# Performance work log

Measured on AMD Instinct MI355X. Metric: run time of the kernel, lower is better.

## Reference

```python
import jax, jax.numpy as jnp
import numpy as np

B, T, H, L, O = 64, 256, 1024, 4, 1024
LN_EPS = 1e-5


def setup_inputs() -> dict:
    key = jax.random.key(0)
    ks = jax.random.split(key, 8)
    s = 1.0 / np.sqrt(H)
    return {
        "inputs": jax.random.normal(ks[0], (B, T, H), jnp.float32),
        "Wx": jax.random.normal(ks[1], (L, H, H), jnp.float32) * s,   # torch Linear weight [out,in]
        "bx": jax.random.normal(ks[2], (L, H), jnp.float32) * s,
        "Wh": jax.random.normal(ks[3], (L, H, H), jnp.float32) * s,   # bias=False
        "ln_g": jnp.ones((L, H), jnp.float32),
        "ln_b": jnp.zeros((L, H), jnp.float32),
        "Wy": jax.random.normal(ks[4], (O, H), jnp.float32) * s,
        "by": jax.random.normal(ks[5], (O,), jnp.float32) * s,
    }


def _layernorm(z, g, b):
    mu = jnp.mean(z, axis=-1, keepdims=True)
    var = jnp.mean(jnp.square(z - mu), axis=-1, keepdims=True)
    return (z - mu) * jax.lax.rsqrt(var + LN_EPS) * g + b


def _forward(inputs, Wx, bx, Wh, ln_g, ln_b, Wy, by):
    x = inputs                                  # [B, T, H]
    n_layers = Wx.shape[0]
    for l in range(n_layers):
        Wx_l, bx_l, Wh_l = Wx[l], bx[l], Wh[l]
        g_l, b_l = ln_g[l], ln_b[l]

        def step(h, x_t):
            # h_t = tanh(LN(x_t Wx^T + bx + h Wh^T))  (dropout off in eval)
            z = x_t @ Wx_l.T + bx_l + h @ Wh_l.T
            h_new = jnp.tanh(_layernorm(z, g_l, b_l))
            return h_new, h_new

        h0 = jnp.zeros((x.shape[0], Wh_l.shape[0]), x.dtype)
        _, hs = jax.lax.scan(step, h0, jnp.swapaxes(x, 0, 1))  # hs: [T, B, H]
        x = jnp.swapaxes(hs, 0, 1)                              # [B, T, H]
    y = x @ Wy.T + by                                           # [B, T, O]
    return x, y


def reference(inputs, Wx, bx, Wh, ln_g, ln_b, Wy, by):
    return _forward(inputs, Wx, bx, Wh, ln_g, ln_b, Wy, by)
```

## Files before the change

### kernel.cpp

```cpp
#include <hip/hip_runtime.h>
#include <stdint.h>

#define B_ 64
#define T_ 256
#define H_ 1024
#define L_ 4
#define O_ 1024
#define LN_EPS 1e-5f
#define RING_Z 4
#define POLL_CAP (1 << 20)

typedef short v8s __attribute__((ext_vector_type(8)));
typedef float v4f __attribute__((ext_vector_type(4)));
typedef unsigned long long u64t;

__device__ __forceinline__ unsigned short f2bf(float f) {
  union { float f; unsigned u; } v; v.f = f;
  unsigned r = (v.u + 0x7FFFu + ((v.u >> 16) & 1u)) >> 16;
  return (unsigned short)r;
}
__device__ __forceinline__ float bf2f(unsigned short u) {
  union { unsigned u; float f; } v; v.u = ((unsigned)u) << 16; return v.f;
}
__device__ __forceinline__ float tanh_fast(float x) {
  float e = __expf(2.0f * x);
  return 1.0f - 2.0f / (e + 1.0f);
}

__device__ __forceinline__ int hswz(int row, int kq) {
  return ((row << 7) + ((kq ^ (kq >> 4) ^ row) & 127)) << 3;
}

__device__ __forceinline__ void poll_ge(const int* p, int v) {
  int it = 0;
  while (__hip_atomic_load(p, __ATOMIC_RELAXED, __HIP_MEMORY_SCOPE_AGENT) < v) {
    __builtin_amdgcn_s_sleep(1);
    if (++it > POLL_CAP) break;
  }
}

__global__ void k_f2b(const float* __restrict__ src, unsigned short* __restrict__ dst, int n4) {
  int i = blockIdx.x * blockDim.x + threadIdx.x;
  int stride = gridDim.x * blockDim.x;
  for (; i < n4; i += stride) {
    float4 v = *(const float4*)(src + 4 * (size_t)i);
    union { unsigned short u[4]; uint2 q; } p;
    p.u[0] = f2bf(v.x); p.u[1] = f2bf(v.y); p.u[2] = f2bf(v.z); p.u[3] = f2bf(v.w);
    *(uint2*)(dst + 4 * (size_t)i) = p.q;
  }
}

__global__ void k_prep_x(const float* __restrict__ in, unsigned short* __restrict__ X) {
  int row = blockIdx.x;
  int b = row >> 8, t = row & 255;
  const float* src = in + (size_t)row * H_;
  unsigned short* dst = X + ((size_t)t * B_ + b) * H_;
  for (int j = threadIdx.x; j < H_ / 4; j += blockDim.x) {
    float4 v = *(const float4*)(src + 4 * j);
    union { unsigned short u[4]; uint2 q; } p;
    p.u[0] = f2bf(v.x); p.u[1] = f2bf(v.y); p.u[2] = f2bf(v.z); p.u[3] = f2bf(v.w);
    *(uint2*)(dst + 4 * j) = p.q;
  }
}

__launch_bounds__(256, 2)
__global__ void k_gemm32(const float* __restrict__ Xf,
                         const unsigned short* __restrict__ Wb,
                         const float* __restrict__ bias,
                         float* __restrict__ Cout) {
  __shared__ short As[128][40];
  __shared__ short Bs[128][40];
  int bm = blockIdx.x >> 3, bn = blockIdx.x & 7;
  int row0 = bm * 128, col0 = bn * 128;
  int tid = threadIdx.x, lane = tid & 63, w = tid >> 6;
  int wm = w >> 1, wn = w & 1;
  int m15 = lane & 15, quad = lane >> 4;
  v4f acc[4][4];
  #pragma unroll
  for (int a = 0; a < 4; ++a)
    #pragma unroll
    for (int b = 0; b < 4; ++b) acc[a][b] = (v4f){0.f, 0.f, 0.f, 0.f};

  int srow = tid >> 1, sseg = tid & 1;
  const float* gA = Xf + (size_t)(row0 + srow) * 1024 + sseg * 16;
  const unsigned short* gB = Wb + (size_t)(col0 + srow) * 1024 + sseg * 16;

  for (int kb = 0; kb < 32; ++kb) {
    float4 f0 = *(const float4*)(gA + kb * 32);
    float4 f1 = *(const float4*)(gA + kb * 32 + 4);
    float4 f2 = *(const float4*)(gA + kb * 32 + 8);
    float4 f3 = *(const float4*)(gA + kb * 32 + 12);
    v8s a0, a1;
    a0[0] = (short)f2bf(f0.x); a0[1] = (short)f2bf(f0.y); a0[2] = (short)f2bf(f0.z); a0[3] = (short)f2bf(f0.w);
    a0[4] = (short)f2bf(f1.x); a0[5] = (short)f2bf(f1.y); a0[6] = (short)f2bf(f1.z); a0[7] = (short)f2bf(f1.w);
    a1[0] = (short)f2bf(f2.x); a1[1] = (short)f2bf(f2.y); a1[2] = (short)f2bf(f2.z); a1[3] = (short)f2bf(f2.w);
    a1[4] = (short)f2bf(f3.x); a1[5] = (short)f2bf(f3.y); a1[6] = (short)f2bf(f3.z); a1[7] = (short)f2bf(f3.w);
    v8s b0 = *(const v8s*)(gB + kb * 32);
    v8s b1 = *(const v8s*)(gB + kb * 32 + 8);
    *(v8s*)&As[srow][sseg * 16]     = a0;
    *(v8s*)&As[srow][sseg * 16 + 8] = a1;
    *(v8s*)&Bs[srow][sseg * 16]     = b0;
    *(v8s*)&Bs[srow][sseg * 16 + 8] = b1;
    __syncthreads();
    v8s af[4], bfr[4];
    #pragma unroll
    for (int mt = 0; mt < 4; ++mt) af[mt]  = *(v8s*)&As[wm * 64 + mt * 16 + m15][quad * 8];
    #pragma unroll
    for (int nt = 0; nt < 4; ++nt) bfr[nt] = *(v8s*)&Bs[wn * 64 + nt * 16 + m15][quad * 8];
    #pragma unroll
    for (int mt = 0; mt < 4; ++mt)
      #pragma unroll
      for (int nt = 0; nt < 4; ++nt)
        acc[mt][nt] = __builtin_amdgcn_mfma_f32_16x16x32_bf16(af[mt], bfr[nt], acc[mt][nt], 0, 0, 0);
    __syncthreads();
  }
  #pragma unroll
  for (int mt = 0; mt < 4; ++mt) {
    #pragma unroll
    for (int nt = 0; nt < 4; ++nt) {
      int col = col0 + wn * 64 + nt * 16 + m15;
      float bv = bias[col];
      #pragma unroll
      for (int r = 0; r < 4; ++r) {
        int row = row0 + wm * 64 + mt * 16 + quad * 4 + r;
        Cout[(size_t)row * 1024 + col] = acc[mt][nt][r] + bv;
      }
    }
  }
}

__launch_bounds__(256, 1)
__global__ void k_fused(const unsigned short* __restrict__ Whb_all,
                        const unsigned short* __restrict__ Wxb_all,
                        const float* __restrict__ bx_all,
                        const float* __restrict__ lng_all,
                        const float* __restrict__ lnb_all,
                        unsigned short* Xl,
                        float* Zr,
                        int* fz,
                        float* __restrict__ outx)
{
  __shared__ short hs[16 * 1024];
  __shared__ float sG[1024], sB[1024];

  const int tid = threadIdx.x, lane = tid & 63, w = tid >> 6;
  const int bid = blockIdx.x;
  const int l = bid >> 6, rb = (bid >> 4) & 3, cb = bid & 15;
  const int r0 = rb * 16, c0 = cb * 64;
  const int m15 = lane & 15, quad = lane >> 4;
  const int myrow = 4 * w + quad;
  const int chunk = m15;
  const int colg = c0 + w * 16 + m15;

  for (int i = tid; i < 1024; i += 256) { sG[i] = lng_all[l * H_ + i]; sB[i] = lnb_all[l * H_ + i]; }

  v8s bh[32];
  {
    const unsigned short* wr = Whb_all + ((size_t)l * H_ + colg) * H_ + quad * 8;
    #pragma unroll
    for (int ks = 0; ks < 32; ++ks) bh[ks] = *(const v8s*)(wr + ks * 32);
  }

  const float bias = bx_all[l * H_ + colg];
  const unsigned short* wxb = Wxb_all + ((size_t)l * H_ + colg) * H_ + quad * 8;
  int* myfz = fz + ((l * 64 + rb * 16 + cb) << 5);
  const int* peer_fz = fz + ((l * 64 + rb * 16 + chunk) << 5);
  const int* prev_fz = (l > 0) ? fz + (((l - 1) * 64 + rb * 16 + chunk) << 5) : (const int*)nullptr;

  const size_t TBH = (size_t)T_ * B_ * H_;
  const unsigned short* Xin = Xl + (size_t)l * TBH;
  unsigned short* Xout = (l < L_ - 1) ? Xl + (size_t)(l + 1) * TBH : (unsigned short*)nullptr;
  float* Zl = Zr + (size_t)l * RING_Z * 4 * 16 * 1024;

  if (l > 0) poll_ge(prev_fz, 2);
  __syncthreads();
  v4f acc = (v4f){bias, bias, bias, bias};
  {
    const unsigned short* xr = Xin + ((size_t)r0 + m15) * H_ + quad * 8;
    #pragma unroll 1
    for (int kb = 0; kb < 4; ++kb) {
      #pragma unroll
      for (int k8 = 0; k8 < 8; ++k8) {
        int ks = kb * 8 + k8;
        v8s a = *(const v8s*)(xr + ks * 32);
        v8s b = *(const v8s*)(wxb + ks * 32);
        acc = __builtin_amdgcn_mfma_f32_16x16x32_bf16(a, b, acc, 0, 0, 0);
      }
    }
  }

  for (int t = 0; t < T_; ++t) {
    float* zo = Zl + (size_t)((t & (RING_Z - 1)) * 4 + rb) * 16 * 1024;
    #pragma unroll
    for (int r = 0; r < 4; ++r)
      __hip_atomic_store(&zo[(size_t)(quad * 4 + r) * H_ + colg], acc[r],
                         __ATOMIC_RELAXED, __HIP_MEMORY_SCOPE_AGENT);
    __syncthreads();
    if (tid == 0)
      __hip_atomic_store(myfz, t + 1, __ATOMIC_RELAXED, __HIP_MEMORY_SCOPE_AGENT);

    if (t < T_ - 1) {
      if (l > 0) poll_ge(prev_fz, t + 3);
      __syncthreads();
      acc = (v4f){bias, bias, bias, bias};
      const unsigned short* xr = Xin + ((size_t)(t + 1) * B_ + r0 + m15) * H_ + quad * 8;
      #pragma unroll 1
      for (int kb = 0; kb < 4; ++kb) {
        #pragma unroll
        for (int k8 = 0; k8 < 8; ++k8) {
          int ks = kb * 8 + k8;
          v8s a = *(const v8s*)(xr + ks * 32);
          v8s b = *(const v8s*)(wxb + ks * 32);
          acc = __builtin_amdgcn_mfma_f32_16x16x32_bf16(a, b, acc, 0, 0, 0);
        }
      }
    }

    poll_ge(peer_fz, t + 1);
    const u64t* zp = (const u64t*)(zo + (size_t)myrow * H_ + chunk * 64);
    float2 zr2[32];
    #pragma unroll
    for (int j = 0; j < 32; ++j) {
      union { u64t u; float2 f; } cv;
      cv.u = __hip_atomic_load(zp + j, __ATOMIC_RELAXED, __HIP_MEMORY_SCOPE_AGENT);
      zr2[j] = cv.f;
    }
    float s = 0.f, s2 = 0.f;
    #pragma unroll
    for (int j = 0; j < 32; ++j) {
      s  += zr2[j].x + zr2[j].y;
      s2 += zr2[j].x * zr2[j].x + zr2[j].y * zr2[j].y;
    }
    #pragma unroll
    for (int m = 1; m < 16; m <<= 1) { s += __shfl_xor(s, m); s2 += __shfl_xor(s2, m); }
    float mu = s * (1.f / 1024.f);
    float var = s2 * (1.f / 1024.f) - mu * mu;
    float rs = rsqrtf(var + LN_EPS);
    #pragma unroll
    for (int g8 = 0; g8 < 8; ++g8) {
      v8s hp;
      #pragma unroll
      for (int e = 0; e < 8; ++e) {
        int cg = chunk * 64 + g8 * 8 + e;
        float zv = (e & 1) ? zr2[g8 * 4 + (e >> 1)].y : zr2[g8 * 4 + (e >> 1)].x;
        float hv = tanh_fast((zv - mu) * rs * sG[cg] + sB[cg]);
        hp[e] = (short)f2bf(hv);
      }
      *(v8s*)&hs[hswz(myrow, chunk * 8 + g8)] = hp;
    }
    __syncthreads();

    {
      int row = tid >> 4, ci = tid & 15;
      int colbase = c0 + ci * 4;
      const short* hp = &hs[hswz(row, colbase >> 3) + (ci & 1) * 4];
      union { unsigned short u[4]; u64t q; } pk;
      pk.u[0] = (unsigned short)hp[0]; pk.u[1] = (unsigned short)hp[1];
      pk.u[2] = (unsigned short)hp[2]; pk.u[3] = (unsigned short)hp[3];
      if (l < L_ - 1) {
        u64t* xdst = (u64t*)(Xout + ((size_t)t * B_ + r0 + row) * H_ + colbase);
        __hip_atomic_store(xdst, pk.q, __ATOMIC_RELAXED, __HIP_MEMORY_SCOPE_AGENT);
      } else {
        float4 f;
        f.x = bf2f(pk.u[0]); f.y = bf2f(pk.u[1]); f.z = bf2f(pk.u[2]); f.w = bf2f(pk.u[3]);
        *(float4*)(outx + ((size_t)(r0 + row) * T_ + t) * H_ + colbase) = f;
      }
    }
    if (t < T_ - 1) {
      #pragma unroll
      for (int ks = 0; ks < 32; ++ks) {
        v8s a = *(const v8s*)&hs[hswz(m15, ks * 4 + quad)];
        acc = __builtin_amdgcn_mfma_f32_16x16x32_bf16(a, bh[ks], acc, 0, 0, 0);
      }
    }
  }
  __syncthreads();
  if (tid == 0)
    __hip_atomic_store(myfz, T_ + 1, __ATOMIC_RELAXED, __HIP_MEMORY_SCOPE_AGENT);
}

extern "C" void kernel_launch(void* const* d_in, const int* in_sizes, int n_in,
                              void* d_out, int out_size, void* d_ws, size_t ws_size,
                              hipStream_t stream) {
  const float* inp = (const float*)d_in[0];
  const float* Wx  = (const float*)d_in[1];
  const float* bx  = (const float*)d_in[2];
  const float* Wh  = (const float*)d_in[3];
  const float* lng = (const float*)d_in[4];
  const float* lnb = (const float*)d_in[5];
  const float* Wy  = (const float*)d_in[6];
  const float* by  = (const float*)d_in[7];
  float* out_x = (float*)d_out;
  float* out_y = out_x + (size_t)B_ * T_ * H_;

  char* ws = (char*)d_ws;
  unsigned short* Whb = (unsigned short*)(ws);
  unsigned short* Wxb = (unsigned short*)(ws + ((size_t)8 << 20));
  unsigned short* Wyb = (unsigned short*)(ws + ((size_t)16 << 20));
  int* fzf            = (int*)(ws + ((size_t)18 << 20));
  float* Zr           = (float*)(ws + ((size_t)19 << 20));
  unsigned short* Xl  = (unsigned short*)(ws + ((size_t)23 << 20));

  hipMemsetAsync(fzf, 0, (size_t)L_ * 64 * 32 * sizeof(int), stream);
  k_f2b<<<1024, 256, 0, stream>>>(Wh, Whb, (L_ * H_ * H_) / 4);
  k_f2b<<<1024, 256, 0, stream>>>(Wx, Wxb, (L_ * H_ * H_) / 4);
  k_f2b<<<256, 256, 0, stream>>>(Wy, Wyb, (O_ * H_) / 4);
  k_prep_x<<<B_ * T_, 256, 0, stream>>>(inp, Xl);

  k_fused<<<256, 256, 0, stream>>>(Whb, Wxb, bx, lng, lnb, Xl, Zr, fzf, out_x);

  k_gemm32<<<1024, 256, 0, stream>>>(out_x, Wyb, by, out_y);
}
```

Before: 5.175 ms.

## Use 8 wide blocks per layer covering all batch rows, staging x in LDS

Each layer now runs on 8 blocks of 512 threads instead of 64 blocks of 256. Each block owns 128 hidden columns for all 64 batch rows, so it only exchanges the pre-norm sums with 8 peers per time step instead of 16. The input tile for the next step is copied into LDS once and shared by all waves for the Wx product, instead of every wave reading it from global memory. The aim is to cut cross-block flag traffic and redundant loads on the latency-bound recurrence. The cost is far fewer active CUs, and each block does eight times more MFMA work and LayerNorm rows per step, with a large dynamic LDS allocation.

```diff
diff --git a/kernel.cpp b/kernel.cpp
--- a/kernel.cpp
+++ b/kernel.cpp
@@ -8,7 +8,10 @@
 #define O_ 1024
 #define LN_EPS 1e-5f
 #define RING_Z 4
+#define G_ 8
+#define WT_ 512
 #define POLL_CAP (1 << 20)
+#define SMEM_BYTES (131072 + 8192)
 
 typedef short v8s __attribute__((ext_vector_type(8)));
 typedef float v4f __attribute__((ext_vector_type(4)));
@@ -129,7 +132,7 @@
   }
 }
 
-__launch_bounds__(256, 1)
+__launch_bounds__(512, 2)
 __global__ void k_fused(const unsigned short* __restrict__ Whb_all,
                         const unsigned short* __restrict__ Wxb_all,
                         const float* __restrict__ bx_all,
@@ -140,19 +143,20 @@
                         int* fz,
                         float* __restrict__ outx)
 {
-  __shared__ short hs[16 * 1024];
-  __shared__ float sG[1024], sB[1024];
+  extern __shared__ char smem[];
+  short* hs = (short*)smem;
+  float* sG = (float*)(smem + 131072);
+  float* sB = sG + 1024;
 
   const int tid = threadIdx.x, lane = tid & 63, w = tid >> 6;
   const int bid = blockIdx.x;
-  const int l = bid >> 6, rb = (bid >> 4) & 3, cb = bid & 15;
-  const int r0 = rb * 16, c0 = cb * 64;
+  const int l = bid >> 3, g = bid & 7;
+  const int c0 = g * 128;
   const int m15 = lane & 15, quad = lane >> 4;
-  const int myrow = 4 * w + quad;
-  const int chunk = m15;
   const int colg = c0 + w * 16 + m15;
-
-  for (int i = tid; i < 1024; i += 256) { sG[i] = lng_all[l * H_ + i]; sB[i] = lnb_all[l * H_ + i]; }
+  const int chunk = tid & 15;
+
+  for (int i = tid; i < 1024; i += WT_) { sG[i] = lng_all[l * H_ + i]; sB[i] = lnb_all[l * H_ + i]; }
 
   v8s bh[32];
   {
@@ -163,114 +167,173 @@
 
   const float bias = bx_all[l * H_ + colg];
   const unsigned short* wxb = Wxb_all + ((size_t)l * H_ + colg) * H_ + quad * 8;
-  int* myfz = fz + ((l * 64 + rb * 16 + cb) << 5);
-  const int* peer_fz = fz + ((l * 64 + rb * 16 + chunk) << 5);
-  const int* prev_fz = (l > 0) ? fz + (((l - 1) * 64 + rb * 16 + chunk) << 5) : (const int*)nullptr;
+
+  int* fzl = fz + ((l * G_) << 5);
+  int* myfz = fzl + (g << 5);
+  const int* peer_fz = fzl + ((chunk >> 1) << 5);
+  const int* prev_fz = (l > 0) ? fz + ((((l - 1) * G_) + (chunk >> 1)) << 5) : (const int*)nullptr;
 
   const size_t TBH = (size_t)T_ * B_ * H_;
   const unsigned short* Xin = Xl + (size_t)l * TBH;
   unsigned short* Xout = (l < L_ - 1) ? Xl + (size_t)(l + 1) * TBH : (unsigned short*)nullptr;
-  float* Zl = Zr + (size_t)l * RING_Z * 4 * 16 * 1024;
+  float* Zl = Zr + (size_t)l * RING_Z * 64 * 1024;
+
+  auto stage_x = [&](int t1) {
+    const int rr = tid >> 4;
+    #pragma unroll
+    for (int hh = 0; hh < 2; ++hh) {
+      const int row = rr + hh * 32;
+      const unsigned short* src = Xin + ((size_t)t1 * B_ + row) * H_ + chunk * 64;
+      #pragma unroll
+      for (int g8 = 0; g8 < 8; ++g8)
+        *(v8s*)&hs[hswz(row, chunk * 8 + g8)] = *(const v8s*)(src + g8 * 8);
+    }
+  };
+
+  v4f acc[4];
 
   if (l > 0) poll_ge(prev_fz, 2);
+  stage_x(0);
   __syncthreads();
-  v4f acc = (v4f){bias, bias, bias, bias};
-  {
-    const unsigned short* xr = Xin + ((size_t)r0 + m15) * H_ + quad * 8;
-    #pragma unroll 1
-    for (int kb = 0; kb < 4; ++kb) {
-      #pragma unroll
-      for (int k8 = 0; k8 < 8; ++k8) {
-        int ks = kb * 8 + k8;
-        v8s a = *(const v8s*)(xr + ks * 32);
-        v8s b = *(const v8s*)(wxb + ks * 32);
-        acc = __builtin_amdgcn_mfma_f32_16x16x32_bf16(a, b, acc, 0, 0, 0);
+  #pragma unroll
+  for (int mt = 0; mt < 4; ++mt) acc[mt] = (v4f){bias, bias, bias, bias};
+  #pragma unroll 1
+  for (int kb = 0; kb < 8; ++kb) {
+    v8s bt[4];
+    #pragma unroll
+    for (int k4 = 0; k4 < 4; ++k4) bt[k4] = *(const v8s*)(wxb + (kb * 4 + k4) * 32);
+    #pragma unroll
+    for (int k4 = 0; k4 < 4; ++k4) {
+      const int ks = kb * 4 + k4;
+      #pragma unroll
+      for (int mt = 0; mt < 4; ++mt) {
+        v8s a = *(const v8s*)&hs[hswz(mt * 16 + m15, ks * 4 + quad)];
+        acc[mt] = __builtin_amdgcn_mfma_f32_16x16x32_bf16(a, bt[k4], acc[mt], 0, 0, 0);
       }
     }
   }
 
   for (int t = 0; t < T_; ++t) {
-    float* zo = Zl + (size_t)((t & (RING_Z - 1)) * 4 + rb) * 16 * 1024;
-    #pragma unroll
-    for (int r = 0; r < 4; ++r)
-      __hip_atomic_store(&zo[(size_t)(quad * 4 + r) * H_ + colg], acc[r],
-                         __ATOMIC_RELAXED, __HIP_MEMORY_SCOPE_AGENT);
+    const bool haveB = (t < T_ - 1);
+    float* zo = Zl + (size_t)(t & (RING_Z - 1)) * 64 * 1024;
+    #pragma unroll
+    for (int mt = 0; mt < 4; ++mt)
+      #pragma unroll
+      for (int r = 0; r < 4; ++r)
+        __hip_atomic_store(&zo[(size_t)(mt * 16 + quad * 4 + r) * H_ + colg], acc[mt][r],
+                           __ATOMIC_RELAXED, __HIP_MEMORY_SCOPE_AGENT);
     __syncthreads();
     if (tid == 0)
       __hip_atomic_store(myfz, t + 1, __ATOMIC_RELAXED, __HIP_MEMORY_SCOPE_AGENT);
 
-    if (t < T_ - 1) {
+    if (haveB) {
       if (l > 0) poll_ge(prev_fz, t + 3);
+      stage_x(t + 1);
+    }
+    __syncthreads();
+    if (haveB) {
+      #pragma unroll
+      for (int mt = 0; mt < 4; ++mt) acc[mt] = (v4f){bias, bias, bias, bias};
+      #pragma unroll 1
+      for (int kb = 0; kb < 8; ++kb) {
+        v8s bt[4];
+        #pragma unroll
+        for (int k4 = 0; k4 < 4; ++k4) bt[k4] = *(const v8s*)(wxb + (kb * 4 + k4) * 32);
+        #pragma unroll
+        for (int k4 = 0; k4 < 4; ++k4) {
+          const int ks = kb * 4 + k4;
+          #pragma unroll
+          for (int mt = 0; mt < 4; ++mt) {
+            v8s a = *(const v8s*)&hs[hswz(mt * 16 + m15, ks * 4 + quad)];
+            acc[mt] = __builtin_amdgcn_mfma_f32_16x16x32_bf16(a, bt[k4], acc[mt], 0, 0, 0);
+          }
+        }
+      }
       __syncthreads();
-      acc = (v4f){bias, bias, bias, bias};
-      const unsigned short* xr = Xin + ((size_t)(t + 1) * B_ + r0 + m15) * H_ + quad * 8;
+    }
+
+    poll_ge(peer_fz, t + 1);
+    #pragma unroll 1
+    for (int half = 0; half < 2; ++half) {
+      const int row = (tid >> 4) + half * 32;
+      float2 zh[32];
+      const u64t* zp = (const u64t*)(zo + (size_t)row * H_ + chunk * 64);
+      #pragma unroll
+      for (int j = 0; j < 32; ++j) {
+        union { u64t u; float2 f; } cv;
+        cv.u = __hip_atomic_load(zp + j, __ATOMIC_RELAXED, __HIP_MEMORY_SCOPE_AGENT);
+        zh[j] = cv.f;
+      }
+      float s = 0.f, s2 = 0.f;
+      #pragma unroll
+      for (int j = 0; j < 32; ++j) {
+        s  += zh[j].x + zh[j].y;
+        s2 += zh[j].x * zh[j].x + zh[j].y * zh[j].y;
+      }
+      #pragma unroll
+      for (int m = 1; m < 16; m <<= 1) { s += __shfl_xor(s, m); s2 += __shfl_xor(s2, m); }
+      float mu = s * (1.f / 1024.f);
+      float var = s2 * (1.f / 1024.f) - mu * mu;
+      float rs = rsqrtf(var + LN_EPS);
+      #pragma unroll
+      for (int g8 = 0; g8 < 8; ++g8) {
+        v8s hp;
+        #pragma unroll
+        for (int e = 0; e < 8; ++e) {
+          int cg = chunk * 64 + g8 * 8 + e;
+          float zv = (e & 1) ? zh[g8 * 4 + (e >> 1)].y : zh[g8 * 4 + (e >> 1)].x;
+          float hv = tanh_fast((zv - mu) * rs * sG[cg] + sB[cg]);
+          hp[e] = (short)f2bf(hv);
+        }
+        *(v8s*)&hs[hswz(row, chunk * 8 + g8)] = hp;
+      }
+    }
+    __syncthreads();
+
+    {
+      const int row = tid >> 3, ci = tid & 7;
+      const int colbase = c0 + ci * 16;
+      const int kq = colbase >> 3;
+      const v8s p0 = *(const v8s*)&hs[hswz(row, kq)];
+      const v8s p1 = *(const v8s*)&hs[hswz(row, kq + 1)];
+      if (l < L_ - 1) {
+        union { unsigned short u[8]; u64t q[2]; } k0, k1;
+        #pragma unroll
+        for (int e = 0; e < 8; ++e) { k0.u[e] = (unsigned short)p0[e]; k1.u[e] = (unsigned short)p1[e]; }
+        u64t* xdst = (u64t*)(Xout + ((size_t)t * B_ + row) * H_ + colbase);
+        __hip_atomic_store(xdst + 0, k0.q[0], __ATOMIC_RELAXED, __HIP_MEMORY_SCOPE_AGENT);
+        __hip_atomic_store(xdst + 1, k0.q[1], __ATOMIC_RELAXED, __HIP_MEMORY_SCOPE_AGENT);
+        __hip_atomic_store(xdst + 2, k1.q[0], __ATOMIC_RELAXED, __HIP_MEMORY_SCOPE_AGENT);
+        __hip_atomic_store(xdst + 3, k1.q[1], __ATOMIC_RELAXED, __HIP_MEMORY_SCOPE_AGENT);
+      } else {
+        float* od = outx + ((size_t)row * T_ + t) * H_ + colbase;
+        float4 f;
+        f.x = bf2f((unsigned short)p0[0]); f.y = bf2f((unsigned short)p0[1]);
+        f.z = bf2f((unsigned short)p0[2]); f.w = bf2f((unsigned short)p0[3]);
+        *(float4*)(od + 0) = f;
+        f.x = bf2f((unsigned short)p0[4]); f.y = bf2f((unsigned short)p0[5]);
+        f.z = bf2f((unsigned short)p0[6]); f.w = bf2f((unsigned short)p0[7]);
+        *(float4*)(od + 4) = f;
+        f.x = bf2f((unsigned short)p1[0]); f.y = bf2f((unsigned short)p1[1]);
+        f.z = bf2f((unsigned short)p1[2]); f.w = bf2f((unsigned short)p1[3]);
+        *(float4*)(od + 8) = f;
+        f.x = bf2f((unsigned short)p1[4]); f.y = bf2f((unsigned short)p1[5]);
+        f.z = bf2f((unsigned short)p1[6]); f.w = bf2f((unsigned short)p1[7]);
+        *(float4*)(od + 12) = f;
+      }
+    }
+    if (haveB) {
       #pragma unroll 1
-      for (int kb = 0; kb < 4; ++kb) {
-        #pragma unroll
-        for (int k8 = 0; k8 < 8; ++k8) {
-          int ks = kb * 8 + k8;
-          v8s a = *(const v8s*)(xr + ks * 32);
-          v8s b = *(const v8s*)(wxb + ks * 32);
-          acc = __builtin_amdgcn_mfma_f32_16x16x32_bf16(a, b, acc, 0, 0, 0);
+      for (int kb = 0; kb < 8; ++kb) {
+        #pragma unroll
+        for (int k4 = 0; k4 < 4; ++k4) {
+          const int ks = kb * 4 + k4;
+          #pragma unroll
+          for (int mt = 0; mt < 4; ++mt) {
+            v8s a = *(const v8s*)&hs[hswz(mt * 16 + m15, ks * 4 + quad)];
+            acc[mt] = __builtin_amdgcn_mfma_f32_16x16x32_bf16(a, bh[ks], acc[mt], 0, 0, 0);
+          }
         }
-      }
-    }
-
-    poll_ge(peer_fz, t + 1);
-    const u64t* zp = (const u64t*)(zo + (size_t)myrow * H_ + chunk * 64);
-    float2 zr2[32];
-    #pragma unroll
-    for (int j = 0; j < 32; ++j) {
-      union { u64t u; float2 f; } cv;
-      cv.u = __hip_atomic_load(zp + j, __ATOMIC_RELAXED, __HIP_MEMORY_SCOPE_AGENT);
-      zr2[j] = cv.f;
-    }
-    float s = 0.f, s2 = 0.f;
-    #pragma unroll
-    for (int j = 0; j < 32; ++j) {
-      s  += zr2[j].x + zr2[j].y;
-      s2 += zr2[j].x * zr2[j].x + zr2[j].y * zr2[j].y;
-    }
-    #pragma unroll
-    for (int m = 1; m < 16; m <<= 1) { s += __shfl_xor(s, m); s2 += __shfl_xor(s2, m); }
-    float mu = s * (1.f / 1024.f);
-    float var = s2 * (1.f / 1024.f) - mu * mu;
-    float rs = rsqrtf(var + LN_EPS);
-    #pragma unroll
-    for (int g8 = 0; g8 < 8; ++g8) {
-      v8s hp;
-      #pragma unroll
-      for (int e = 0; e < 8; ++e) {
-        int cg = chunk * 64 + g8 * 8 + e;
-        float zv = (e & 1) ? zr2[g8 * 4 + (e >> 1)].y : zr2[g8 * 4 + (e >> 1)].x;
-        float hv = tanh_fast((zv - mu) * rs * sG[cg] + sB[cg]);
-        hp[e] = (short)f2bf(hv);
-      }
-      *(v8s*)&hs[hswz(myrow, chunk * 8 + g8)] = hp;
-    }
-    __syncthreads();
-
-    {
-      int row = tid >> 4, ci = tid & 15;
-      int colbase = c0 + ci * 4;
-      const short* hp = &hs[hswz(row, colbase >> 3) + (ci & 1) * 4];
-      union { unsigned short u[4]; u64t q; } pk;
-      pk.u[0] = (unsigned short)hp[0]; pk.u[1] = (unsigned short)hp[1];
-      pk.u[2] = (unsigned short)hp[2]; pk.u[3] = (unsigned short)hp[3];
-      if (l < L_ - 1) {
-        u64t* xdst = (u64t*)(Xout + ((size_t)t * B_ + r0 + row) * H_ + colbase);
-        __hip_atomic_store(xdst, pk.q, __ATOMIC_RELAXED, __HIP_MEMORY_SCOPE_AGENT);
-      } else {
-        float4 f;
-        f.x = bf2f(pk.u[0]); f.y = bf2f(pk.u[1]); f.z = bf2f(pk.u[2]); f.w = bf2f(pk.u[3]);
-        *(float4*)(outx + ((size_t)(r0 + row) * T_ + t) * H_ + colbase) = f;
-      }
-    }
-    if (t < T_ - 1) {
-      #pragma unroll
-      for (int ks = 0; ks < 32; ++ks) {
-        v8s a = *(const v8s*)&hs[hswz(m15, ks * 4 + quad)];
-        acc = __builtin_amdgcn_mfma_f32_16x16x32_bf16(a, bh[ks], acc, 0, 0, 0);
       }
     }
   }
@@ -301,13 +364,21 @@
   float* Zr           = (float*)(ws + ((size_t)19 << 20));
   unsigned short* Xl  = (unsigned short*)(ws + ((size_t)23 << 20));
 
-  hipMemsetAsync(fzf, 0, (size_t)L_ * 64 * 32 * sizeof(int), stream);
+  static bool s_attr = false;
+  if (!s_attr) {
+    hipFuncSetAttribute(reinterpret_cast<const void*>(k_fused),
+                        hipFuncAttributeMaxDynamicSharedMemorySize, SMEM_BYTES);
+    s_attr = true;
+  }
+
+  hipMemsetAsync(fzf, 0, (size_t)L_ * G_ * 32 * sizeof(int), stream);
   k_f2b<<<1024, 256, 0, stream>>>(Wh, Whb, (L_ * H_ * H_) / 4);
   k_f2b<<<1024, 256, 0, stream>>>(Wx, Wxb, (L_ * H_ * H_) / 4);
   k_f2b<<<256, 256, 0, stream>>>(Wy, Wyb, (O_ * H_) / 4);
   k_prep_x<<<B_ * T_, 256, 0, stream>>>(inp, Xl);
 
-  k_fused<<<256, 256, 0, stream>>>(Whb, Wxb, bx, lng, lnb, Xl, Zr, fzf, out_x);
+  k_fused<<<L_ * G_, WT_, SMEM_BYTES, stream>>>(Whb, Wxb, bx, lng, lnb,
+                                                Xl, Zr, fzf, out_x);
 
   k_gemm32<<<1024, 256, 0, stream>>>(out_x, Wyb, by, out_y);
 }
```

Measured after the change: 14.87 ms. 187% more time.
